# Kernel tuning notes

Hardware: AMD Instinct MI355X
Metric: run time of the kernel (lower is better)

Reference implementation:

```python
import jax, jax.numpy as jnp
import numpy as np

B, IN, HID, H = 8192, 1024, 2048, 8
UP = 2 * IN          # input_size * proj_factor
HS = HID // H        # head size = 256
EPS = 1e-5


def _blockdiag(x, w, b):
    # x: [B, UP] -> chunk into H blocks of UP//H, per-block linear to HID//H
    xb = x.reshape(B, H, UP // H)
    y = jnp.einsum('bhi,hio->bho', xb, w)
    return y.reshape(B, HID) + b


def setup_inputs() -> dict:
    key = jax.random.key(0)
    ks = jax.random.split(key, 20)
    rn = lambda k, s: jax.random.normal(k, s, jnp.float32)
    p = lambda k, *s: rn(k, s) * 0.02
    return dict(
        x=rn(ks[0], (B, IN)),
        h_prev=rn(ks[1], (B, HID)), c_prev=rn(ks[2], (B, HID)),
        n_prev=rn(ks[3], (B, HID)), m_prev=rn(ks[4], (B, HID)),
        ln_g=jnp.ones(IN), ln_b=jnp.zeros(IN),
        w_ul=p(ks[5], IN, UP), b_ul=jnp.zeros(UP),
        w_ur=p(ks[6], IN, HID), b_ur=jnp.zeros(HID),
        conv_w=p(ks[7], 4), conv_b=jnp.zeros(()),
        w_skip=p(ks[8], UP, HID), b_skip=jnp.zeros(HID),
        w_q=p(ks[9], H, UP // H, HID // H), b_q=jnp.zeros(HID),
        w_k=p(ks[10], H, UP // H, HID // H), b_k=jnp.zeros(HID),
        w_v=p(ks[11], H, UP // H, HID // H), b_v=jnp.zeros(HID),
        w_i=p(ks[12], UP, HID), b_i=jnp.zeros(HID),
        w_f=p(ks[13], UP, HID), b_f=jnp.zeros(HID),
        w_o=p(ks[14], UP, HID), b_o=jnp.zeros(HID),
        gn_g=jnp.ones(HID), gn_b=jnp.zeros(HID),
        w_down=p(ks[15], HID, IN), b_down=jnp.zeros(IN),
    )


def reference(x, h_prev, c_prev, n_prev, m_prev, ln_g, ln_b,
              w_ul, b_ul, w_ur, b_ur, conv_w, conv_b, w_skip, b_skip,
              w_q, b_q, w_k, b_k, w_v, b_v, w_i, b_i, w_f, b_f, w_o, b_o,
              gn_g, gn_b, w_down, b_down):
    # LayerNorm over features
    mu = x.mean(-1, keepdims=True)
    var = x.var(-1, keepdims=True)
    xn = (x - mu) * jax.lax.rsqrt(var + EPS) * ln_g + ln_b

    xul = xn @ w_ul + b_ul          # [B, UP]
    xur = xn @ w_ur + b_ur          # [B, HID]

    # causal conv1d (kernel 4, 1 channel) along the feature axis, left-pad 3
    xp = jnp.pad(xul, ((0, 0), (3, 0)))
    xc = conv_b + sum(conv_w[j] * xp[:, j:j + UP] for j in range(4))
    xc = jax.nn.silu(xc)            # [B, UP]

    x_skip = xc @ w_skip + b_skip

    q = _blockdiag(xc, w_q, b_q)
    k = _blockdiag(xc, w_k, b_k) / np.sqrt(HS).astype(np.float32)
    v = _blockdiag(xul, w_v, b_v)

    i_t = xc @ w_i + b_i
    f_t = xc @ w_f + b_f
    o = jax.nn.sigmoid(xul @ w_o + b_o)

    m_t = jnp.maximum(f_t + m_prev, i_t)
    i = jnp.exp(i_t - m_t)
    f = jnp.exp(f_t + m_prev - m_t)
    c_t = f * c_prev + i * (v * k)
    n_t = f * n_prev + i * k

    denom = jnp.max(jnp.abs(n_t.T @ q), axis=1)     # [HID]
    h_t = o * (c_t * q) / denom

    # GroupNorm on (N, C), groups = H
    hg = h_t.reshape(B, H, HID // H)
    gm = hg.mean(-1, keepdims=True)
    gv = hg.var(-1, keepdims=True)
    hn = ((hg - gm) * jax.lax.rsqrt(gv + EPS)).reshape(B, HID) * gn_g + gn_b

    out = (hn + x_skip) * jax.nn.silu(xur)
    return out @ w_down + b_down + x, h_t, c_t, n_t, m_t
```

## Files before the change

kernel.cpp:

```cpp
#include <hip/hip_runtime.h>
#include <stdint.h>

#define B_    8192
#define IN_   1024
#define HID_  2048
#define UP_   2048
#define H_    8
#define HS_   256
#define EPS_  1e-5f

typedef __bf16 bf16x8 __attribute__((ext_vector_type(8)));
typedef float f32x4 __attribute__((ext_vector_type(4)));
typedef unsigned short u16x4 __attribute__((ext_vector_type(4)));
typedef unsigned short u16x8 __attribute__((ext_vector_type(8)));

__device__ __forceinline__ unsigned short f2bf(float f) {
  union { float f; unsigned int u; } v; v.f = f;
  unsigned int u = v.u;
  unsigned int r = (u + 0x7fffu + ((u >> 16) & 1u)) >> 16;
  return (unsigned short)r;
}
__device__ __forceinline__ float bf2f(unsigned short h) {
  union { unsigned int u; float f; } v; v.u = ((unsigned int)h) << 16;
  return v.f;
}

__device__ __forceinline__ void gload_lds16(const void* g, void* l) {
  auto gp = reinterpret_cast<const uint32_t __attribute__((address_space(1)))*>(
      reinterpret_cast<uintptr_t>(g));
  auto lp = reinterpret_cast<uint32_t __attribute__((address_space(3)))*>(
      reinterpret_cast<uintptr_t>(l));
  __builtin_amdgcn_global_load_lds(gp, lp, 16, 0, 0);
}

#define PREFETCH_AF(DST, BASE, MI0)                                         \
  DST[0][0] = *(const bf16x8*)((BASE) + (aRdBase + (MI0) * 2048));          \
  DST[0][1] = *(const bf16x8*)((BASE) + ((aRdBase + (MI0) * 2048) ^ 64));   \
  DST[1][0] = *(const bf16x8*)((BASE) + (aRdBase + ((MI0) + 1) * 2048));    \
  DST[1][1] = *(const bf16x8*)((BASE) + ((aRdBase + ((MI0) + 1) * 2048) ^ 64));

#define MFMA_CLUSTER(AF, Q)                                                 \
  _Pragma("unroll")                                                         \
  for (int kq = 0; kq < 2; ++kq)                                            \
    _Pragma("unroll")                                                       \
    for (int m2 = 0; m2 < 2; ++m2)                                          \
      _Pragma("unroll")                                                     \
      for (int ni = 0; ni < 4; ++ni)                                        \
        acc[(Q) * 2 + m2][ni] = __builtin_amdgcn_mfma_f32_16x16x32_bf16(    \
            AF[m2][kq], bfr[ni][kq], acc[(Q) * 2 + m2][ni], 0, 0, 0);

template <typename OutT, bool HAS_ADD>
__global__ __launch_bounds__(512, 2) void gemm8p(
    const unsigned short* __restrict__ A, int lda, int a_zoff,
    const unsigned short* __restrict__ W, int ldw, int w_zoff,
    const float* __restrict__ bias, const float* __restrict__ bias2,
    int bias_zoff,
    OutT* __restrict__ C, OutT* __restrict__ C2, int ldc, int c_zoff,
    int c_split,
    const float* __restrict__ ADD, float scale, float scale2, int K)
{
  __shared__ char lds[163840];
  const int z = blockIdx.z;
  A += (size_t)z * a_zoff;
  W += (size_t)z * w_zoff;
  if (bias) bias += (size_t)z * bias_zoff;
  if (bias2) bias2 += (size_t)z * bias_zoff;

  const int nwg = gridDim.x * gridDim.y;
  const int orig = blockIdx.y * gridDim.x + blockIdx.x;
  const int q8 = nwg >> 3, r8 = nwg & 7;
  const int xcd = orig & 7, xi = orig >> 3;
  const int wg = (xcd < r8 ? xcd * (q8 + 1) : r8 * (q8 + 1) + (xcd - r8) * q8) + xi;
  const int bx = wg % gridDim.x, by = wg / gridDim.x;

  const int t = threadIdx.x;
  const int lane = t & 63, wave = t >> 6;
  const int wr = wave >> 2, wc = wave & 3;
  const int l15 = lane & 15, l4 = lane >> 4;
  const int row0 = by * 256, col0 = bx * 256;

  const int lrow = lane >> 3;
  const int lslot = (lane & 7) ^ lrow;
  const size_t aLane = (size_t)lrow * lda * 2 + (size_t)lslot * 16;
  const size_t wLane = (size_t)lrow * ldw * 2 + (size_t)lslot * 16;
  const char* Abase = (const char*)A;
  const char* Wbase = (const char*)W;

  const int aRdBase = (wr * 128 + l15) * 128 + (((l4) ^ (l15 & 7)) * 16);
  const int bRdBase = (wc * 64 + l15) * 128 + (((l4) ^ (l15 & 7)) * 16);

  auto issueA = [&](int abuf, int half, int tile) {
#pragma unroll
    for (int j = 0; j < 2; ++j) {
      const int rbase = half * 128 + j * 64 + wave * 8;
      gload_lds16(Abase + (size_t)(row0 + rbase) * (lda * 2) + (size_t)tile * 128 + aLane,
                  lds + abuf * 32768 + rbase * 128 + lane * 16);
    }
  };
  auto issueB = [&](int bbuf, int half, int tile) {
#pragma unroll
    for (int j = 0; j < 2; ++j) {
      const int rbase = half * 128 + j * 64 + wave * 8;
      gload_lds16(Wbase + (size_t)(col0 + rbase) * (ldw * 2) + (size_t)tile * 128 + wLane,
                  lds + 98304 + bbuf * 32768 + rbase * 128 + lane * 16);
    }
  };

  f32x4 acc[8][4] = {};
  const int NT = K >> 6;

  bf16x8 bfr[4][2];
  bf16x8 afA[2][2], afB[2][2];

  issueA(0, 0, 0); issueA(0, 1, 0);
  issueB(0, 0, 0); issueB(0, 1, 0);
  if (NT > 1) {
    issueA(1, 0, 1); issueA(1, 1, 1);
    issueB(1, 0, 1); issueB(1, 1, 1);
    asm volatile("s_waitcnt vmcnt(8)" ::: "memory");
  } else {
    asm volatile("s_waitcnt vmcnt(0)" ::: "memory");
  }
  __builtin_amdgcn_s_barrier();
  __builtin_amdgcn_sched_barrier(0);
  {
    const char* ldsA0 = lds;
    PREFETCH_AF(afA, ldsA0, 0)
  }

  for (int T = 0; T < NT; ++T) {
    const char* ldsA = lds + (T % 3) * 32768;
    const char* ldsAn = lds + ((T + 1) % 3) * 32768;
    const char* ldsB = lds + 98304 + (T & 1) * 32768;
    const int abufN = (T + 2) % 3;
    const int bbufN = T & 1;
#pragma unroll
    for (int q = 0; q < 4; ++q) {
      if (q == 3) {
        if (T + 2 < NT) asm volatile("s_waitcnt vmcnt(6)" ::: "memory");
        else            asm volatile("s_waitcnt vmcnt(0)" ::: "memory");
      }
      if (q == 0 && T + 2 < NT) issueA(abufN, 0, T + 2);
      if (q == 1 && T + 2 < NT) issueA(abufN, 1, T + 2);
      if (q == 2 && T + 2 < NT) issueB(bbufN, 0, T + 2);
      if (q == 3 && T + 2 < NT) issueB(bbufN, 1, T + 2);
      __builtin_amdgcn_s_barrier();
      if (q == 0) {
#pragma unroll
        for (int ni = 0; ni < 4; ++ni) {
          bfr[ni][0] = *(const bf16x8*)(ldsB + (bRdBase + ni * 2048));
          bfr[ni][1] = *(const bf16x8*)(ldsB + ((bRdBase + ni * 2048) ^ 64));
        }
      }
      asm volatile("s_waitcnt lgkmcnt(0)" ::: "memory");
      __builtin_amdgcn_sched_barrier(0);
      if (q == 0) { PREFETCH_AF(afB, ldsA, 2) }
      else if (q == 1) { PREFETCH_AF(afA, ldsA, 4) }
      else if (q == 2) { PREFETCH_AF(afB, ldsA, 6) }
      else if (T + 1 < NT) { PREFETCH_AF(afA, ldsAn, 0) }
      __builtin_amdgcn_s_setprio(1);
      if ((q & 1) == 0) { MFMA_CLUSTER(afA, q) }
      else              { MFMA_CLUSTER(afB, q) }
      __builtin_amdgcn_s_setprio(0);
      __builtin_amdgcn_s_barrier();
      __builtin_amdgcn_sched_barrier(0);
    }
  }

  const float* bp = bias;
  OutT* Cp = C;
  int cbase = col0;
  float sc = scale;
  if (col0 >= c_split) { bp = bias2; Cp = C2; cbase = col0 - c_split; sc = scale2; }
#pragma unroll
  for (int mi = 0; mi < 8; ++mi) {
#pragma unroll
    for (int ni = 0; ni < 4; ++ni) {
#pragma unroll
      for (int r = 0; r < 4; ++r) {
        const int m = row0 + wr * 128 + mi * 16 + l4 * 4 + r;
        const int n = wc * 64 + ni * 16 + l15;
        float v = acc[mi][ni][r];
        if (bp) v += bp[cbase + n];
        v *= sc;
        const size_t ci = (size_t)m * ldc + (size_t)z * c_zoff + cbase + n;
        if constexpr (HAS_ADD) v += ADD[ci];
        if constexpr (sizeof(OutT) == 2) Cp[ci] = (OutT)f2bf(v);
        else Cp[ci] = v;
      }
    }
  }
}

__global__ __launch_bounds__(256) void denom_reduce(
    const float* __restrict__ part, float* __restrict__ denom)
{
  const int m = blockIdx.x, t = threadIdx.x;
  const size_t P = (size_t)HID_ * HID_;
  float v = 0.f;
  for (int n = t; n < HID_; n += 256) {
    const size_t o = (size_t)m * HID_ + n;
    float s = part[o] + part[P + o] + part[2 * P + o] + part[3 * P + o];
    v = fmaxf(v, fabsf(s));
  }
#pragma unroll
  for (int off = 1; off < 64; off <<= 1) v = fmaxf(v, __shfl_xor(v, off, 64));
  __shared__ float red[4];
  if ((t & 63) == 0) red[t >> 6] = v;
  __syncthreads();
  if (t == 0) denom[m] = fmaxf(fmaxf(red[0], red[1]), fmaxf(red[2], red[3]));
}

__global__ __launch_bounds__(256) void down_reduce(
    const float* __restrict__ part, const float* __restrict__ x,
    const float* __restrict__ bias, float* __restrict__ out)
{
  const size_t idx = ((size_t)blockIdx.x * 256 + threadIdx.x) * 4;
  const size_t P = (size_t)B_ * IN_;
  f32x4 a = *(const f32x4*)(part + idx);
  f32x4 b = *(const f32x4*)(part + P + idx);
  f32x4 xv = *(const f32x4*)(x + idx);
  const int j = (int)(idx & (IN_ - 1));
  f32x4 bv = *(const f32x4*)(bias + j);
  f32x4 o;
#pragma unroll
  for (int e = 0; e < 4; ++e) o[e] = a[e] + b[e] + bv[e] + xv[e];
  *(f32x4*)(out + idx) = o;
}

template <typename InT>
__global__ __launch_bounds__(256) void transpose_bf(
    const InT* __restrict__ in, unsigned short* __restrict__ out, int R, int C,
    int izoff, int ozoff)
{
  __shared__ float tile[32][33];
  in += (size_t)blockIdx.z * izoff;
  out += (size_t)blockIdx.z * ozoff;
  const int cb = blockIdx.x * 32, rb = blockIdx.y * 32;
  const int tx = threadIdx.x, ty = threadIdx.y;
  for (int i = ty; i < 32; i += 8) {
    InT v = in[(size_t)(rb + i) * C + cb + tx];
    float f;
    if constexpr (sizeof(InT) == 2) f = bf2f((unsigned short)v);
    else f = (float)v;
    tile[i][tx] = f;
  }
  __syncthreads();
  for (int i = ty; i < 32; i += 8)
    out[(size_t)(cb + i) * R + rb + tx] = f2bf(tile[tx][i]);
}

__global__ __launch_bounds__(256) void ln_kernel(
    const float* __restrict__ x, const float* __restrict__ g,
    const float* __restrict__ b, unsigned short* __restrict__ xn)
{
  const int brow = blockIdx.x, t = threadIdx.x;
  const int lane = t & 63, wave = t >> 6;
  const float* xr = x + (size_t)brow * IN_;
  f32x4 v = *(const f32x4*)(xr + t * 4);
  float s = v[0] + v[1] + v[2] + v[3];
  float q = v[0]*v[0] + v[1]*v[1] + v[2]*v[2] + v[3]*v[3];
#pragma unroll
  for (int off = 32; off; off >>= 1) {
    s += __shfl_xor(s, off, 64);
    q += __shfl_xor(q, off, 64);
  }
  __shared__ float ss[4], sq[4];
  if (lane == 0) { ss[wave] = s; sq[wave] = q; }
  __syncthreads();
  s = ss[0] + ss[1] + ss[2] + ss[3];
  q = sq[0] + sq[1] + sq[2] + sq[3];
  const float mean = s * (1.f / IN_);
  const float var = q * (1.f / IN_) - mean * mean;
  const float rs = rsqrtf(var + EPS_);
  u16x4 o;
#pragma unroll
  for (int e = 0; e < 4; ++e) {
    const int j = t * 4 + e;
    o[e] = f2bf((v[e] - mean) * rs * g[j] + b[j]);
  }
  *(u16x4*)(xn + (size_t)brow * IN_ + t * 4) = o;
}

__global__ __launch_bounds__(256) void conv_kernel(
    const unsigned short* __restrict__ xul, const float* __restrict__ cw,
    const float* __restrict__ cb, unsigned short* __restrict__ xc)
{
  const int brow = blockIdx.x, t = threadIdx.x;
  const size_t base = (size_t)brow * UP_;
  const int j0 = t * 8;
  float xv[11];
#pragma unroll
  for (int e = 0; e < 11; ++e) {
    const int j = j0 + e - 3;
    xv[e] = (j >= 0) ? bf2f(xul[base + j]) : 0.f;
  }
  const float w0 = cw[0], w1 = cw[1], w2 = cw[2], w3 = cw[3], bb = cb[0];
  u16x8 o;
#pragma unroll
  for (int e = 0; e < 8; ++e) {
    float sv = bb + w0 * xv[e] + w1 * xv[e + 1] + w2 * xv[e + 2] + w3 * xv[e + 3];
    o[e] = f2bf(sv / (1.f + expf(-sv)));
  }
  *(u16x8*)(xc + base + j0) = o;
}

__global__ __launch_bounds__(256) void gates_kernel(
    const unsigned short* __restrict__ sif,
    const unsigned short* __restrict__ kb, const unsigned short* __restrict__ vb,
    const float* __restrict__ mprev, const float* __restrict__ cprev,
    const float* __restrict__ nprev,
    float* __restrict__ mo, float* __restrict__ co, float* __restrict__ no,
    unsigned short* __restrict__ nT)
{
  __shared__ unsigned short nt_t[64][72];
  const int t = threadIdx.x;
  const int r = t >> 2, cq = t & 3;
  const int row = blockIdx.y * 64 + r;
  const int colb = blockIdx.x * 64 + cq * 16;
  const size_t hidb = (size_t)row * HID_ + colb;
  const size_t sifb = (size_t)row * 6144 + colb;
#pragma unroll
  for (int e4 = 0; e4 < 4; ++e4) {
    const int c4 = e4 * 4;
    f32x4 mp = *(const f32x4*)(mprev + hidb + c4);
    f32x4 cp = *(const f32x4*)(cprev + hidb + c4);
    f32x4 np = *(const f32x4*)(nprev + hidb + c4);
    u16x4 iv = *(const u16x4*)(sif + sifb + 2048 + c4);
    u16x4 fv = *(const u16x4*)(sif + sifb + 4096 + c4);
    u16x4 kv = *(const u16x4*)(kb + hidb + c4);
    u16x4 vv = *(const u16x4*)(vb + hidb + c4);
    f32x4 mo4, co4, no4;
#pragma unroll
    for (int e = 0; e < 4; ++e) {
      const float ft = bf2f(fv[e]) + mp[e];
      const float it = bf2f(iv[e]);
      const float mt = fmaxf(ft, it);
      const float ie = expf(it - mt);
      const float fe = expf(ft - mt);
      const float k = bf2f(kv[e]), v = bf2f(vv[e]);
      mo4[e] = mt;
      co4[e] = fe * cp[e] + ie * (v * k);
      no4[e] = fe * np[e] + ie * k;
      nt_t[r][cq * 16 + c4 + e] = f2bf(no4[e]);
    }
    *(f32x4*)(mo + hidb + c4) = mo4;
    *(f32x4*)(co + hidb + c4) = co4;
    *(f32x4*)(no + hidb + c4) = no4;
  }
  __syncthreads();
  const int cT = t >> 2, sq = t & 3;
  u16x8 o0, o1;
#pragma unroll
  for (int e = 0; e < 8; ++e) {
    o0[e] = nt_t[sq * 16 + e][cT];
    o1[e] = nt_t[sq * 16 + 8 + e][cT];
  }
  const size_t ob = (size_t)(blockIdx.x * 64 + cT) * B_ + blockIdx.y * 64 + sq * 16;
  *(u16x8*)(nT + ob) = o0;
  *(u16x8*)(nT + ob + 8) = o1;
}

__global__ __launch_bounds__(256) void hgn_kernel(
    const float* __restrict__ ct, const unsigned short* __restrict__ olin,
    const unsigned short* __restrict__ qb, const float* __restrict__ denom,
    const unsigned short* __restrict__ sif, const unsigned short* __restrict__ xurb,
    const float* __restrict__ gng, const float* __restrict__ gnb,
    float* __restrict__ ho, unsigned short* __restrict__ pre)
{
  const int brow = blockIdx.x, t = threadIdx.x;
  const size_t base = (size_t)brow * HID_ + t * 8;
  u16x8 ov = *(const u16x8*)(olin + base);
  u16x8 qv = *(const u16x8*)(qb + base);
  f32x4 c0 = *(const f32x4*)(ct + base);
  f32x4 c1 = *(const f32x4*)(ct + base + 4);
  float h[8];
  float s = 0.f, sq = 0.f;
#pragma unroll
  for (int e = 0; e < 8; ++e) {
    const float o = 1.f / (1.f + expf(-bf2f(ov[e])));
    const float cv = (e < 4) ? c0[e] : c1[e - 4];
    const float hv = o * cv * bf2f(qv[e]) / denom[t * 8 + e];
    h[e] = hv; s += hv; sq += hv * hv;
  }
#pragma unroll
  for (int e = 0; e < 8; ++e) ho[base + e] = h[e];
#pragma unroll
  for (int off = 1; off < 32; off <<= 1) {
    s += __shfl_xor(s, off, 64);
    sq += __shfl_xor(sq, off, 64);
  }
  const float mean = s * (1.f / HS_);
  const float var = sq * (1.f / HS_) - mean * mean;
  const float rs = rsqrtf(var + EPS_);
  u16x8 sv = *(const u16x8*)(sif + (size_t)brow * 6144 + t * 8);
  u16x8 xv = *(const u16x8*)(xurb + base);
  u16x8 pv;
#pragma unroll
  for (int e = 0; e < 8; ++e) {
    const int j = t * 8 + e;
    const float hn = (h[e] - mean) * rs * gng[j] + gnb[j];
    const float xr = bf2f(xv[e]);
    const float sil = xr / (1.f + expf(-xr));
    pv[e] = f2bf((hn + bf2f(sv[e])) * sil);
  }
  *(u16x8*)(pre + base) = pv;
}

extern "C" void kernel_launch(void* const* d_in, const int* in_sizes, int n_in,
                              void* d_out, int out_size, void* d_ws, size_t ws_size,
                              hipStream_t stream)
{
  const float* x      = (const float*)d_in[0];
  const float* c_prev = (const float*)d_in[2];
  const float* n_prev = (const float*)d_in[3];
  const float* m_prev = (const float*)d_in[4];
  const float* ln_g   = (const float*)d_in[5];
  const float* ln_b   = (const float*)d_in[6];
  const float* w_ul   = (const float*)d_in[7];
  const float* b_ul   = (const float*)d_in[8];
  const float* w_ur   = (const float*)d_in[9];
  const float* b_ur   = (const float*)d_in[10];
  const float* conv_w = (const float*)d_in[11];
  const float* conv_b = (const float*)d_in[12];
  const float* w_skip = (const float*)d_in[13];
  const float* b_skip = (const float*)d_in[14];
  const float* w_q    = (const float*)d_in[15];
  const float* b_q    = (const float*)d_in[16];
  const float* w_k    = (const float*)d_in[17];
  const float* b_k    = (const float*)d_in[18];
  const float* w_v    = (const float*)d_in[19];
  const float* b_v    = (const float*)d_in[20];
  const float* w_i    = (const float*)d_in[21];
  const float* b_i    = (const float*)d_in[22];
  const float* w_f    = (const float*)d_in[23];
  const float* b_f    = (const float*)d_in[24];
  const float* w_o    = (const float*)d_in[25];
  const float* b_o    = (const float*)d_in[26];
  const float* gn_g   = (const float*)d_in[27];
  const float* gn_b   = (const float*)d_in[28];
  const float* w_down = (const float*)d_in[29];
  const float* b_down = (const float*)d_in[30];

  float* out_p = (float*)d_out;
  float* h_p = out_p + (size_t)B_ * IN_;
  float* c_p = h_p + (size_t)B_ * HID_;
  float* n_p = c_p + (size_t)B_ * HID_;
  float* m_p = n_p + (size_t)B_ * HID_;

  char* ws = (char*)d_ws;
  size_t off = 0;
  auto alloc = [&](size_t n) -> void* {
    void* p = ws + off;
    off += (n + 255) & ~(size_t)255;
    return p;
  };

  const size_t BH2 = (size_t)B_ * HID_ * 2;

  unsigned short* xn_bf   = (unsigned short*)alloc((size_t)B_ * IN_ * 2);
  unsigned short* xul_bf  = (unsigned short*)alloc(BH2);
  unsigned short* xur_bf  = (unsigned short*)alloc(BH2);
  unsigned short* xc_bf   = (unsigned short*)alloc(BH2);
  unsigned short* sif_bf  = (unsigned short*)alloc((size_t)B_ * 6144 * 2);
  unsigned short* q_bf    = (unsigned short*)alloc(BH2);
  unsigned short* k_bf    = (unsigned short*)alloc(BH2);
  unsigned short* v_bf    = (unsigned short*)alloc(BH2);
  unsigned short* olin_bf = (unsigned short*)alloc(BH2);
  unsigned short* qT_bf   = (unsigned short*)alloc(BH2);
  unsigned short* nT_bf   = (unsigned short*)alloc(BH2);
  unsigned short* pre_bf  = (unsigned short*)alloc(BH2);
  float* denom = (float*)alloc(HID_ * sizeof(float));
  float* part  = (float*)alloc((size_t)4 * HID_ * HID_ * sizeof(float));
  float* b_sif = (float*)alloc(6144 * sizeof(float));
  unsigned short* wt_ulur = (unsigned short*)alloc((size_t)4096 * IN_ * 2);
  unsigned short* wt_sif  = (unsigned short*)alloc((size_t)6144 * UP_ * 2);
  unsigned short* wt_qk   = (unsigned short*)alloc((size_t)H_ * 512 * HS_ * 2);
  unsigned short* wt_v    = (unsigned short*)alloc((size_t)H_ * HS_ * HS_ * 2);
  unsigned short* wt_o    = (unsigned short*)alloc((size_t)UP_ * HID_ * 2);
  unsigned short* wt_down = (unsigned short*)alloc((size_t)HID_ * IN_ * 2);

  if (off > ws_size) return;

  const dim3 tb32(32, 8);
  const int NOSPLIT = 1 << 30;

  hipMemcpyAsync(b_sif, b_skip, 2048 * 4, hipMemcpyDeviceToDevice, stream);
  hipMemcpyAsync(b_sif + 2048, b_i, 2048 * 4, hipMemcpyDeviceToDevice, stream);
  hipMemcpyAsync(b_sif + 4096, b_f, 2048 * 4, hipMemcpyDeviceToDevice, stream);

  transpose_bf<float><<<dim3(64, 32, 1), tb32, 0, stream>>>(w_ul, wt_ulur, 1024, 2048, 0, 0);
  transpose_bf<float><<<dim3(64, 32, 1), tb32, 0, stream>>>(w_ur, wt_ulur + (size_t)2048 * 1024, 1024, 2048, 0, 0);
  transpose_bf<float><<<dim3(64, 64, 1), tb32, 0, stream>>>(w_skip, wt_sif, 2048, 2048, 0, 0);
  transpose_bf<float><<<dim3(64, 64, 1), tb32, 0, stream>>>(w_i, wt_sif + (size_t)2048 * 2048, 2048, 2048, 0, 0);
  transpose_bf<float><<<dim3(64, 64, 1), tb32, 0, stream>>>(w_f, wt_sif + (size_t)4096 * 2048, 2048, 2048, 0, 0);
  transpose_bf<float><<<dim3(8, 8, 8), tb32, 0, stream>>>(w_q, wt_qk, 256, 256, 65536, 131072);
  transpose_bf<float><<<dim3(8, 8, 8), tb32, 0, stream>>>(w_k, wt_qk + 65536, 256, 256, 65536, 131072);
  transpose_bf<float><<<dim3(8, 8, 8), tb32, 0, stream>>>(w_v, wt_v, 256, 256, 65536, 65536);
  transpose_bf<float><<<dim3(64, 64, 1), tb32, 0, stream>>>(w_o, wt_o, 2048, 2048, 0, 0);
  transpose_bf<float><<<dim3(32, 64, 1), tb32, 0, stream>>>(w_down, wt_down, 2048, 1024, 0, 0);

  ln_kernel<<<B_, 256, 0, stream>>>(x, ln_g, ln_b, xn_bf);

  gemm8p<unsigned short, false><<<dim3(16, 32, 1), 512, 0, stream>>>(
      xn_bf, IN_, 0, wt_ulur, IN_, 0, b_ul, b_ur, 0,
      xul_bf, xur_bf, HID_, 0, 2048, nullptr, 1.f, 1.f, IN_);

  conv_kernel<<<B_, 256, 0, stream>>>(xul_bf, conv_w, conv_b, xc_bf);

  gemm8p<unsigned short, false><<<dim3(24, 32, 1), 512, 0, stream>>>(
      xc_bf, UP_, 0, wt_sif, UP_, 0, b_sif, nullptr, 0,
      sif_bf, sif_bf, 6144, 0, NOSPLIT, nullptr, 1.f, 1.f, UP_);

  gemm8p<unsigned short, false><<<dim3(2, 32, 8), 512, 0, stream>>>(
      xc_bf, UP_, HS_, wt_qk, HS_, 512 * HS_, b_q, b_k, HS_,
      q_bf, k_bf, HID_, HS_, 256, nullptr, 1.f, 0.0625f, HS_);

  gemm8p<unsigned short, false><<<dim3(1, 32, 8), 512, 0, stream>>>(
      xul_bf, UP_, HS_, wt_v, HS_, HS_ * HS_, b_v, nullptr, HS_,
      v_bf, v_bf, HID_, HS_, NOSPLIT, nullptr, 1.f, 1.f, HS_);

  gemm8p<unsigned short, false><<<dim3(8, 32, 1), 512, 0, stream>>>(
      xul_bf, UP_, 0, wt_o, UP_, 0, b_o, nullptr, 0,
      olin_bf, olin_bf, HID_, 0, NOSPLIT, nullptr, 1.f, 1.f, UP_);

  gates_kernel<<<dim3(HID_ / 64, B_ / 64, 1), 256, 0, stream>>>(
      sif_bf, k_bf, v_bf, m_prev, c_prev, n_prev, m_p, c_p, n_p, nT_bf);

  transpose_bf<unsigned short><<<dim3(64, 256, 1), tb32, 0, stream>>>(
      q_bf, qT_bf, B_, HID_, 0, 0);

  gemm8p<float, false><<<dim3(8, 8, 4), 512, 0, stream>>>(
      nT_bf, B_, B_ / 4, qT_bf, B_, B_ / 4, nullptr, nullptr, 0,
      part, part, HID_, HID_ * HID_, NOSPLIT, nullptr, 1.f, 1.f, B_ / 4);
  denom_reduce<<<HID_, 256, 0, stream>>>(part, denom);

  hgn_kernel<<<B_, 256, 0, stream>>>(
      c_p, olin_bf, q_bf, denom, sif_bf, xur_bf, gn_g, gn_b, h_p, pre_bf);

  gemm8p<float, false><<<dim3(4, 32, 2), 512, 0, stream>>>(
      pre_bf, UP_, 1024, wt_down, UP_, 1024, nullptr, nullptr, 0,
      part, part, IN_, B_ * IN_, NOSPLIT, nullptr, 1.f, 1.f, 1024);
  down_reduce<<<(B_ * IN_ / 4) / 256, 256, 0, stream>>>(part, x, b_down, out_p);
}
```

Measured before the change: 1.026 ms.

## Restructure GEMM main loop to cut barriers and overlap LDS reads with MFMA

Rewrites the unrolled per-quarter loop of the bf16 GEMM so it uses two workgroup barriers per K-tile instead of eight. The loop now relies on partial lgkmcnt waits, so LDS fragment reads for the next cluster overlap with the current MFMA cluster. The B fragments and the first A fragments for the next tile are loaded at the end of each iteration. Global-to-LDS issue is regrouped and the vmcnt threshold changed, which risks race hazards on the triple and double buffers if the counts are wrong.

```diff
diff --git a/kernel.cpp b/kernel.cpp
--- a/kernel.cpp
+++ b/kernel.cpp
@@ -33,13 +33,23 @@
   __builtin_amdgcn_global_load_lds(gp, lp, 16, 0, 0);
 }
 
+#define SB0 __builtin_amdgcn_sched_barrier(0)
+
 #define PREFETCH_AF(DST, BASE, MI0)                                         \
   DST[0][0] = *(const bf16x8*)((BASE) + (aRdBase + (MI0) * 2048));          \
   DST[0][1] = *(const bf16x8*)((BASE) + ((aRdBase + (MI0) * 2048) ^ 64));   \
   DST[1][0] = *(const bf16x8*)((BASE) + (aRdBase + ((MI0) + 1) * 2048));    \
   DST[1][1] = *(const bf16x8*)((BASE) + ((aRdBase + ((MI0) + 1) * 2048) ^ 64));
 
+#define LOAD_BFR(BASE)                                                      \
+  _Pragma("unroll")                                                         \
+  for (int ni = 0; ni < 4; ++ni) {                                          \
+    bfr[ni][0] = *(const bf16x8*)((BASE) + (bRdBase + ni * 2048));          \
+    bfr[ni][1] = *(const bf16x8*)((BASE) + ((bRdBase + ni * 2048) ^ 64));   \
+  }
+
 #define MFMA_CLUSTER(AF, Q)                                                 \
+  __builtin_amdgcn_s_setprio(1);                                           \
   _Pragma("unroll")                                                         \
   for (int kq = 0; kq < 2; ++kq)                                            \
     _Pragma("unroll")                                                       \
@@ -47,7 +57,8 @@
       _Pragma("unroll")                                                     \
       for (int ni = 0; ni < 4; ++ni)                                        \
         acc[(Q) * 2 + m2][ni] = __builtin_amdgcn_mfma_f32_16x16x32_bf16(    \
-            AF[m2][kq], bfr[ni][kq], acc[(Q) * 2 + m2][ni], 0, 0, 0);
+            AF[m2][kq], bfr[ni][kq], acc[(Q) * 2 + m2][ni], 0, 0, 0);       \
+  __builtin_amdgcn_s_setprio(0);
 
 template <typename OutT, bool HAS_ADD>
 __global__ __launch_bounds__(512, 2) void gemm8p(
@@ -121,50 +132,51 @@
   } else {
     asm volatile("s_waitcnt vmcnt(0)" ::: "memory");
   }
+  SB0;
+  {
+    const char* a0 = lds;
+    const char* b0 = lds + 98304;
+    LOAD_BFR(b0)
+    PREFETCH_AF(afA, a0, 0)
+    PREFETCH_AF(afB, a0, 2)
+  }
   __builtin_amdgcn_s_barrier();
-  __builtin_amdgcn_sched_barrier(0);
-  {
-    const char* ldsA0 = lds;
-    PREFETCH_AF(afA, ldsA0, 0)
-  }
+  SB0;
 
   for (int T = 0; T < NT; ++T) {
     const char* ldsA = lds + (T % 3) * 32768;
-    const char* ldsAn = lds + ((T + 1) % 3) * 32768;
-    const char* ldsB = lds + 98304 + (T & 1) * 32768;
     const int abufN = (T + 2) % 3;
     const int bbufN = T & 1;
-#pragma unroll
-    for (int q = 0; q < 4; ++q) {
-      if (q == 3) {
-        if (T + 2 < NT) asm volatile("s_waitcnt vmcnt(6)" ::: "memory");
-        else            asm volatile("s_waitcnt vmcnt(0)" ::: "memory");
-      }
-      if (q == 0 && T + 2 < NT) issueA(abufN, 0, T + 2);
-      if (q == 1 && T + 2 < NT) issueA(abufN, 1, T + 2);
-      if (q == 2 && T + 2 < NT) issueB(bbufN, 0, T + 2);
-      if (q == 3 && T + 2 < NT) issueB(bbufN, 1, T + 2);
-      __builtin_amdgcn_s_barrier();
-      if (q == 0) {
-#pragma unroll
-        for (int ni = 0; ni < 4; ++ni) {
-          bfr[ni][0] = *(const bf16x8*)(ldsB + (bRdBase + ni * 2048));
-          bfr[ni][1] = *(const bf16x8*)(ldsB + ((bRdBase + ni * 2048) ^ 64));
-        }
-      }
-      asm volatile("s_waitcnt lgkmcnt(0)" ::: "memory");
-      __builtin_amdgcn_sched_barrier(0);
-      if (q == 0) { PREFETCH_AF(afB, ldsA, 2) }
-      else if (q == 1) { PREFETCH_AF(afA, ldsA, 4) }
-      else if (q == 2) { PREFETCH_AF(afB, ldsA, 6) }
-      else if (T + 1 < NT) { PREFETCH_AF(afA, ldsAn, 0) }
-      __builtin_amdgcn_s_setprio(1);
-      if ((q & 1) == 0) { MFMA_CLUSTER(afA, q) }
-      else              { MFMA_CLUSTER(afB, q) }
-      __builtin_amdgcn_s_setprio(0);
-      __builtin_amdgcn_s_barrier();
-      __builtin_amdgcn_sched_barrier(0);
+    asm volatile("s_waitcnt lgkmcnt(4)" ::: "memory"); SB0;
+    MFMA_CLUSTER(afA, 0)
+    PREFETCH_AF(afA, ldsA, 4)
+    if (T + 2 < NT) issueA(abufN, 0, T + 2);
+    asm volatile("s_waitcnt lgkmcnt(4)" ::: "memory"); SB0;
+    MFMA_CLUSTER(afB, 1)
+    __builtin_amdgcn_s_barrier();
+    SB0;
+    PREFETCH_AF(afB, ldsA, 6)
+    if (T + 2 < NT) {
+      issueA(abufN, 1, T + 2);
+      issueB(bbufN, 0, T + 2);
+      issueB(bbufN, 1, T + 2);
     }
+    asm volatile("s_waitcnt lgkmcnt(4)" ::: "memory"); SB0;
+    MFMA_CLUSTER(afA, 2)
+    asm volatile("s_waitcnt lgkmcnt(0)" ::: "memory"); SB0;
+    MFMA_CLUSTER(afB, 3)
+    if (T + 2 < NT) asm volatile("s_waitcnt vmcnt(8)" ::: "memory");
+    else            asm volatile("s_waitcnt vmcnt(0)" ::: "memory");
+    SB0;
+    if (T + 1 < NT) {
+      const char* aN = lds + ((T + 1) % 3) * 32768;
+      const char* bN = lds + 98304 + ((T + 1) & 1) * 32768;
+      LOAD_BFR(bN)
+      PREFETCH_AF(afA, aN, 0)
+      PREFETCH_AF(afB, aN, 2)
+    }
+    __builtin_amdgcn_s_barrier();
+    SB0;
   }
 
   const float* bp = bias;
```

New measurement: 992.8 us. 1.03x faster.
